# Kernel optimization log

Hardware: AMD Instinct MI355X
Metric: run time of the kernel (lower is better)

## Reference

```python
import jax, jax.numpy as jnp
import numpy as np
from jax import lax

NLAT_IN, NLON_IN = 480, 960
NLAT_OUT, NLON_OUT = 721, 1440
KSIZE = 9      # morlet basis: prod(kernel_shape) = 3*3
NNZ = 20       # sparse quadrature entries per output latitude row
C_IN, C_OUT = 32, 32
BATCH = 1


def setup_inputs() -> dict:
    key = jax.random.key(0)
    k1, k2, k3, k4, k5 = jax.random.split(key, 5)
    x = jax.random.normal(k1, (BATCH, C_IN, NLAT_IN, NLON_IN), dtype=jnp.float32)
    weight = jax.random.normal(k2, (C_OUT, C_IN, KSIZE), dtype=jnp.float32) * 0.05
    # sparse DISCO quadrature values (quadrature weights folded in)
    psi_vals = jax.random.uniform(k3, (KSIZE, NLAT_OUT, NNZ), dtype=jnp.float32) / NNZ
    # geodesic neighborhood: latitude rows within +-2 of output row, small lon offsets
    ho = jnp.arange(NLAT_OUT, dtype=jnp.int32)[:, None]
    psi_hi = jnp.clip(ho + jax.random.randint(k4, (NLAT_OUT, NNZ), -2, 3, dtype=jnp.int32), 0, NLAT_OUT - 1)
    psi_dw = jax.random.randint(k5, (NLAT_OUT, NNZ), -10, 11, dtype=jnp.int32) % NLON_OUT
    return {"x": x, "weight": weight, "psi_vals": psi_vals, "psi_hi": psi_hi, "psi_dw": psi_dw}


def _resample_s2(x, h_out, w_out):
    """Bilinear lat interpolation + periodic linear lon interpolation (ResampleS2)."""
    b, c, h, w = x.shape
    # latitude: both grids are linspace(0, pi, nlat) equiangular
    pos_h = jnp.linspace(0.0, float(h - 1), h_out)
    h0 = jnp.clip(jnp.floor(pos_h).astype(jnp.int32), 0, h - 2)
    fh = (pos_h - h0.astype(jnp.float32)).astype(x.dtype)
    x = x[:, :, h0, :] * (1.0 - fh)[None, None, :, None] + x[:, :, h0 + 1, :] * fh[None, None, :, None]
    # longitude: periodic, lon_j = 2*pi*j/nlon
    pos_w = jnp.arange(w_out, dtype=jnp.float32) * (w / w_out)
    w0 = jnp.floor(pos_w).astype(jnp.int32)
    fw = (pos_w - w0.astype(jnp.float32)).astype(x.dtype)
    w0 = w0 % w
    w1 = (w0 + 1) % w
    return x[..., w0] * (1.0 - fw) + x[..., w1] * fw


def _disco_conv(x, weight, psi_vals, psi_hi, psi_dw):
    """Sparse discrete-continuous spherical conv (gather -> basis weight -> channel mix).
    psi is stored for longitude 0 and applied with a periodic longitude shift."""
    b, c, h, w = x.shape  # [B, Cin, 721, 1440]
    o = weight.shape[0]
    wo = jnp.arange(w, dtype=jnp.int32)

    def body(acc, inp):
        v, hi, dw = inp  # v: [K, Hout], hi/dw: [Hout]
        cols = (dw[:, None] + wo[None, :]) % w          # [Hout, W]
        g = x[:, :, hi[:, None], cols]                  # gather -> [B, Cin, Hout, W]
        weff = jnp.einsum("ock,kh->och", weight, v)     # fold basis into channel mix
        return acc + jnp.einsum("och,bchw->bohw", weff, g), None

    acc0 = jnp.zeros((b, o, h, w), dtype=x.dtype)
    scan_in = (jnp.moveaxis(psi_vals, 2, 0), psi_hi.T, psi_dw.T)  # leading axis NNZ
    acc, _ = lax.scan(body, acc0, scan_in)
    return acc


def reference(x, weight, psi_vals, psi_hi, psi_dw):
    x = _resample_s2(x, NLAT_OUT, NLON_OUT)
    return _disco_conv(x, weight, psi_vals, psi_hi, psi_dw)
```

## Files before the change

### kernel.cpp

```cpp
#include <hip/hip_runtime.h>
#include <hip/hip_bf16.h>

#define NLAT_IN  480
#define NLON_IN  960
#define NLAT_OUT 721
#define NLON_OUT 1440
#define KSIZE    9
#define NNZ      20
#define CH       32

typedef __bf16 bf16x8 __attribute__((ext_vector_type(8)));
typedef float  f32x4  __attribute__((ext_vector_type(4)));

__device__ __forceinline__ unsigned short f2bf(float f) {
    unsigned u = __float_as_uint(f);
    u += 0x7fffu + ((u >> 16) & 1u);
    return (unsigned short)(u >> 16);
}

#define W_TILE   180
#define IN_LD4   31
#define LDS_PITCH 129

__global__ __launch_bounds__(256) void resample_kernel(
        const float* __restrict__ x,
        unsigned short* __restrict__ xr) {
    __shared__ float ld[2 * CH * LDS_PITCH];

    int h  = blockIdx.y;
    int bx = blockIdx.x;
    int wb = bx * W_TILE;
    int base_in = bx * (W_TILE * 2 / 3);

    float pos_h = (float)h * (479.0f / 720.0f);
    int h0 = (int)floorf(pos_h);
    if (h0 < 0) h0 = 0;
    if (h0 > NLAT_IN - 2) h0 = NLAT_IN - 2;
    float fh = pos_h - (float)h0;

    const int t = threadIdx.x;
    for (int i = 0; i < 8; ++i) {
        int lin = i * 256 + t;
        if (lin < 2 * CH * IN_LD4) {
            int r   = lin / (CH * IN_LD4);
            int rem = lin - r * (CH * IN_LD4);
            int c   = rem / IN_LD4;
            int j   = rem - c * IN_LD4;
            int src = base_in + 4 * j;
            if (src >= NLON_IN) src -= NLON_IN;
            f32x4 v = *(const f32x4*)(x + ((size_t)c * NLAT_IN + h0 + r) * NLON_IN + src);
            float* dst = ld + (r * CH + c) * LDS_PITCH + 4 * j;
            dst[0] = v.x; dst[1] = v.y; dst[2] = v.z; dst[3] = v.w;
        }
    }
    __syncthreads();

    float ifh = 1.0f - fh;
    for (int i = 0; i < 12; ++i) {
        int d = i * 256 + t;
        if (d >= W_TILE * (CH / 2)) break;
        int w_l   = d >> 4;
        int cpair = d & 15;
        int c = cpair * 2;
        int w = wb + w_l;
        float pos_w = (float)w * ((float)NLON_IN / (float)NLON_OUT);
        int w0 = (int)floorf(pos_w);
        float fw = pos_w - (float)w0;
        int wl0 = w0 - base_in;
        float ifw = 1.0f - fw;

        const float* r0 = ld + c * LDS_PITCH + wl0;
        const float* r1 = r0 + CH * LDS_PITCH;
        float v0 = ifh * (ifw * r0[0] + fw * r0[1]) + fh * (ifw * r1[0] + fw * r1[1]);
        const float* q0 = r0 + LDS_PITCH;
        const float* q1 = r1 + LDS_PITCH;
        float v1 = ifh * (ifw * q0[0] + fw * q0[1]) + fh * (ifw * q1[0] + fw * q1[1]);

        ((unsigned*)xr)[((size_t)h * NLON_OUT + w) * (CH / 2) + cpair] =
            (unsigned)f2bf(v0) | ((unsigned)f2bf(v1) << 16);
    }
}

__global__ __launch_bounds__(256) void weff_kernel(
        const float* __restrict__ weight,
        const float* __restrict__ psi_vals,
        unsigned short* __restrict__ weff) {
    __shared__ float wl[KSIZE * CH * CH];

    const int t = threadIdx.x;
    for (int i = 0; i < 9; ++i) {
        int lin = i * 256 + t;
        if (lin < KSIZE * CH * CH / 4) {
            f32x4 v = *(const f32x4*)(weight + lin * 4);
            float vv[4] = {v.x, v.y, v.z, v.w};
#pragma unroll
            for (int q = 0; q < 4; ++q) {
                int l4 = lin * 4 + q;
                int k  = l4 % KSIZE;
                int occ = l4 / KSIZE;
                wl[k * (CH * CH) + occ] = vv[q];
            }
        }
    }
    __syncthreads();

    int hnz = blockIdx.x * 16 + (t >> 4);
    int cp  = t & 15;
    if (hnz >= NLAT_OUT * NNZ) return;

    float p[KSIZE];
#pragma unroll
    for (int k = 0; k < KSIZE; ++k)
        p[k] = psi_vals[(size_t)k * (NLAT_OUT * NNZ) + hnz];

    unsigned* outp = (unsigned*)weff + (size_t)hnz * (CH * CH / 2) + cp;
#pragma unroll 4
    for (int oc = 0; oc < CH; ++oc) {
        float a0 = 0.f, a1 = 0.f;
        const float* wb = wl + oc * CH + cp * 2;
#pragma unroll
        for (int k = 0; k < KSIZE; ++k) {
            a0 += wb[k * (CH * CH)]     * p[k];
            a1 += wb[k * (CH * CH) + 1] * p[k];
        }
        outp[oc * 16] = (unsigned)f2bf(a0) | ((unsigned)f2bf(a1) << 16);
    }
}

#define ST_ROWS 6
#define ST_COLS 128
#define HBLK2   361
#define NPAIR   (HBLK2 * 15)
#define PER_XCD ((NPAIR + 7) / 8)

__global__ __launch_bounds__(256, 3) void disco_kernel(
        const unsigned short* __restrict__ xr,
        const unsigned short* __restrict__ weff,
        const int* __restrict__ psi_hi,
        const int* __restrict__ psi_dw,
        float* __restrict__ out) {
    __shared__ unsigned short st[ST_ROWS * ST_COLS * CH];

    int bid = blockIdx.x;
    int xcd = bid & 7;
    int p   = xcd * PER_XCD + (bid >> 3);
    if (p >= NPAIR) return;
    int hblk = p / 15;
    int wblk = p - hblk * 15;
    int h0        = hblk * 2;
    int wbase_blk = wblk * 96;

    int wave = threadIdx.x >> 6;
    int lane = threadIdx.x & 63;
    int l15  = lane & 15;
    int quad = lane >> 4;
    int c0   = quad * 8;
    int jh   = wave >> 1;
    int wq   = wave & 1;

    int cstart = wbase_blk - 16;
    if (cstart < 0) cstart += NLON_OUT;
    for (int i = wave; i < ST_ROWS * (ST_COLS / 16); i += 4) {
        int r  = i >> 3;
        int ck = i & 7;
        int gh = h0 - 2 + r;
        gh = gh < 0 ? 0 : (gh > NLAT_OUT - 1 ? NLAT_OUT - 1 : gh);
        int gc = cstart + ck * 16;
        if (gc >= NLON_OUT) gc -= NLON_OUT;
        const unsigned short* gp = xr + ((size_t)gh * NLON_OUT + gc) * CH + lane * 8;
        unsigned short* lp = st + (r * ST_COLS + ck * 16) * CH;
        __builtin_amdgcn_global_load_lds(
            (const __attribute__((address_space(1))) void*)gp,
            (__attribute__((address_space(3))) void*)lp, 16, 0, 0);
    }
    __syncthreads();

    int h = h0 + jh;
    if (h < NLAT_OUT) {
        f32x4 acc[2][3] = {};
        const unsigned short* weff_h = weff + (size_t)h * (NNZ * CH * CH);
        const int* hip_ = psi_hi + h * NNZ;
        const int* dwp  = psi_dw + h * NNZ;
        int wcol0 = 16 + wq * 48 + l15;

#pragma unroll 2
        for (int nz = 0; nz < NNZ; ++nz) {
            int hi = hip_[nz];
            int dw = dwp[nz];
            int shift = dw > 720 ? dw - NLON_OUT : dw;
            int rloc  = hi - h0 + 2;
            const unsigned short* wf = weff_h + nz * (CH * CH);
            bf16x8 a0 = *(const bf16x8*)(wf + l15 * CH + c0);
            bf16x8 a1 = *(const bf16x8*)(wf + (16 + l15) * CH + c0);
            const unsigned short* srow = st + (size_t)rloc * (ST_COLS * CH);
            int cbase = wcol0 + shift;
#pragma unroll
            for (int s = 0; s < 3; ++s) {
                bf16x8 b = *(const bf16x8*)(srow + (cbase + s * 16) * CH + c0);
                acc[0][s] = __builtin_amdgcn_mfma_f32_16x16x32_bf16(a0, b, acc[0][s], 0, 0, 0);
                acc[1][s] = __builtin_amdgcn_mfma_f32_16x16x32_bf16(a1, b, acc[1][s], 0, 0, 0);
            }
        }

#pragma unroll
        for (int hh = 0; hh < 2; ++hh)
#pragma unroll
            for (int s = 0; s < 3; ++s)
#pragma unroll
                for (int r = 0; r < 4; ++r) {
                    int oc = hh * 16 + quad * 4 + r;
                    int w  = wbase_blk + wq * 48 + s * 16 + l15;
                    out[((size_t)oc * NLAT_OUT + h) * NLON_OUT + w] = acc[hh][s][r];
                }
    }
}

extern "C" void kernel_launch(void* const* d_in, const int* in_sizes, int n_in,
                              void* d_out, int out_size, void* d_ws, size_t ws_size,
                              hipStream_t stream) {
    const float* x        = (const float*)d_in[0];
    const float* weight   = (const float*)d_in[1];
    const float* psi_vals = (const float*)d_in[2];
    const int*   psi_hi   = (const int*)d_in[3];
    const int*   psi_dw   = (const int*)d_in[4];
    float* out = (float*)d_out;

    unsigned short* xr = (unsigned short*)d_ws;
    unsigned short* wf = (unsigned short*)((char*)d_ws + (size_t)NLAT_OUT * NLON_OUT * CH * 2);

    {
        dim3 grid(NLON_OUT / W_TILE, NLAT_OUT);
        resample_kernel<<<grid, 256, 0, stream>>>(x, xr);
    }
    {
        int nblk = (NLAT_OUT * NNZ + 15) / 16;
        weff_kernel<<<nblk, 256, 0, stream>>>(weight, psi_vals, wf);
    }
    {
        disco_kernel<<<8 * PER_XCD, 256, 0, stream>>>(xr, wf, psi_hi, psi_dw, out);
    }
}
```

Measured before the change: 316.5 us.

## Widen disco tiles to four rows, swizzle LDS, prefetch weff, vectorize resample stores

The disco kernel now processes four output latitude rows per block using 512 threads. Its staged halo grows from 6 to 8 rows, so each staged input row is reused by more output rows. LDS staging uses an XOR swizzle on column-group offsets to cut bank conflicts on the B-operand reads. Weff fragments and psi indices are software-prefetched two iterations ahead with the nz loop fully unrolled. The resample kernel writes 16-byte vectors of eight channels per thread instead of 4-byte pairs. The trade-off is more registers and LDS per block, which may lower occupancy.

```diff
diff --git a/kernel.cpp b/kernel.cpp
--- a/kernel.cpp
+++ b/kernel.cpp
@@ -11,6 +11,7 @@
 
 typedef __bf16 bf16x8 __attribute__((ext_vector_type(8)));
 typedef float  f32x4  __attribute__((ext_vector_type(4)));
+typedef unsigned u32x4 __attribute__((ext_vector_type(4)));
 
 __device__ __forceinline__ unsigned short f2bf(float f) {
     unsigned u = __float_as_uint(f);
@@ -56,12 +57,11 @@
     __syncthreads();
 
     float ifh = 1.0f - fh;
-    for (int i = 0; i < 12; ++i) {
+    for (int i = 0; i < 3; ++i) {
         int d = i * 256 + t;
-        if (d >= W_TILE * (CH / 2)) break;
-        int w_l   = d >> 4;
-        int cpair = d & 15;
-        int c = cpair * 2;
+        if (d >= W_TILE * (CH / 8)) break;
+        int w_l = d >> 2;
+        int cg  = d & 3;
         int w = wb + w_l;
         float pos_w = (float)w * ((float)NLON_IN / (float)NLON_OUT);
         int w0 = (int)floorf(pos_w);
@@ -69,15 +69,20 @@
         int wl0 = w0 - base_in;
         float ifw = 1.0f - fw;
 
-        const float* r0 = ld + c * LDS_PITCH + wl0;
-        const float* r1 = r0 + CH * LDS_PITCH;
-        float v0 = ifh * (ifw * r0[0] + fw * r0[1]) + fh * (ifw * r1[0] + fw * r1[1]);
-        const float* q0 = r0 + LDS_PITCH;
-        const float* q1 = r1 + LDS_PITCH;
-        float v1 = ifh * (ifw * q0[0] + fw * q0[1]) + fh * (ifw * q1[0] + fw * q1[1]);
-
-        ((unsigned*)xr)[((size_t)h * NLON_OUT + w) * (CH / 2) + cpair] =
-            (unsigned)f2bf(v0) | ((unsigned)f2bf(v1) << 16);
+        unsigned rr[4];
+#pragma unroll
+        for (int j = 0; j < 4; ++j) {
+            int c = cg * 8 + j * 2;
+            const float* r0 = ld + c * LDS_PITCH + wl0;
+            const float* r1 = r0 + CH * LDS_PITCH;
+            float v0 = ifh * (ifw * r0[0] + fw * r0[1]) + fh * (ifw * r1[0] + fw * r1[1]);
+            const float* q0 = r0 + LDS_PITCH;
+            const float* q1 = r1 + LDS_PITCH;
+            float v1 = ifh * (ifw * q0[0] + fw * q0[1]) + fh * (ifw * q1[0] + fw * q1[1]);
+            rr[j] = (unsigned)f2bf(v0) | ((unsigned)f2bf(v1) << 16);
+        }
+        u32x4 uv; uv[0] = rr[0]; uv[1] = rr[1]; uv[2] = rr[2]; uv[3] = rr[3];
+        *(u32x4*)((unsigned*)xr + ((size_t)h * NLON_OUT + w) * (CH / 2) + cg * 4) = uv;
     }
 }
 
@@ -127,13 +132,13 @@
     }
 }
 
-#define ST_ROWS 6
+#define ST_ROWS 8
 #define ST_COLS 128
-#define HBLK2   361
-#define NPAIR   (HBLK2 * 15)
-#define PER_XCD ((NPAIR + 7) / 8)
-
-__global__ __launch_bounds__(256, 3) void disco_kernel(
+#define HBLK4   181
+#define NPAIRD  (HBLK4 * 15)
+#define PER_XCD ((NPAIRD + 7) / 8)
+
+__global__ __launch_bounds__(512, 4) void disco_kernel(
         const unsigned short* __restrict__ xr,
         const unsigned short* __restrict__ weff,
         const int* __restrict__ psi_hi,
@@ -144,10 +149,10 @@
     int bid = blockIdx.x;
     int xcd = bid & 7;
     int p   = xcd * PER_XCD + (bid >> 3);
-    if (p >= NPAIR) return;
+    if (p >= NPAIRD) return;
     int hblk = p / 15;
     int wblk = p - hblk * 15;
-    int h0        = hblk * 2;
+    int h0        = hblk * 4;
     int wbase_blk = wblk * 96;
 
     int wave = threadIdx.x >> 6;
@@ -158,16 +163,38 @@
     int jh   = wave >> 1;
     int wq   = wave & 1;
 
+    int  h  = h0 + jh;
+    bool hv = (h < NLAT_OUT);
+
+    int swz = ((lane >> 2) << 5) + (((lane & 3) ^ ((lane >> 3) & 3)) << 3);
+
+    const unsigned short* weff_h = weff + (size_t)h * (NNZ * CH * CH);
+    const int* hip_ = psi_hi + h * NNZ;
+    const int* dwp  = psi_dw + h * NNZ;
+
+    bf16x8 pa0[2], pa1[2];
+    int phi[2], pdw[2];
+    if (hv) {
+#pragma unroll
+        for (int q = 0; q < 2; ++q) {
+            const unsigned short* wp = weff_h + q * (CH * CH);
+            pa0[q] = *(const bf16x8*)(wp + l15 * CH + c0);
+            pa1[q] = *(const bf16x8*)(wp + (16 + l15) * CH + c0);
+            phi[q] = hip_[q];
+            pdw[q] = dwp[q];
+        }
+    }
+
     int cstart = wbase_blk - 16;
     if (cstart < 0) cstart += NLON_OUT;
-    for (int i = wave; i < ST_ROWS * (ST_COLS / 16); i += 4) {
+    for (int i = wave; i < ST_ROWS * (ST_COLS / 16); i += 8) {
         int r  = i >> 3;
         int ck = i & 7;
         int gh = h0 - 2 + r;
         gh = gh < 0 ? 0 : (gh > NLAT_OUT - 1 ? NLAT_OUT - 1 : gh);
         int gc = cstart + ck * 16;
         if (gc >= NLON_OUT) gc -= NLON_OUT;
-        const unsigned short* gp = xr + ((size_t)gh * NLON_OUT + gc) * CH + lane * 8;
+        const unsigned short* gp = xr + ((size_t)gh * NLON_OUT + gc) * CH + swz;
         unsigned short* lp = st + (r * ST_COLS + ck * 16) * CH;
         __builtin_amdgcn_global_load_lds(
             (const __attribute__((address_space(1))) void*)gp,
@@ -175,28 +202,33 @@
     }
     __syncthreads();
 
-    int h = h0 + jh;
-    if (h < NLAT_OUT) {
+    if (hv) {
         f32x4 acc[2][3] = {};
-        const unsigned short* weff_h = weff + (size_t)h * (NNZ * CH * CH);
-        const int* hip_ = psi_hi + h * NNZ;
-        const int* dwp  = psi_dw + h * NNZ;
         int wcol0 = 16 + wq * 48 + l15;
 
-#pragma unroll 2
+#pragma unroll
         for (int nz = 0; nz < NNZ; ++nz) {
-            int hi = hip_[nz];
-            int dw = dwp[nz];
+            const int sl = nz & 1;
+            bf16x8 a0 = pa0[sl];
+            bf16x8 a1 = pa1[sl];
+            int hi = phi[sl];
+            int dw = pdw[sl];
+            if (nz + 2 < NNZ) {
+                const unsigned short* wp = weff_h + (nz + 2) * (CH * CH);
+                pa0[sl] = *(const bf16x8*)(wp + l15 * CH + c0);
+                pa1[sl] = *(const bf16x8*)(wp + (16 + l15) * CH + c0);
+                phi[sl] = hip_[nz + 2];
+                pdw[sl] = dwp[nz + 2];
+            }
             int shift = dw > 720 ? dw - NLON_OUT : dw;
             int rloc  = hi - h0 + 2;
-            const unsigned short* wf = weff_h + nz * (CH * CH);
-            bf16x8 a0 = *(const bf16x8*)(wf + l15 * CH + c0);
-            bf16x8 a1 = *(const bf16x8*)(wf + (16 + l15) * CH + c0);
-            const unsigned short* srow = st + (size_t)rloc * (ST_COLS * CH);
             int cbase = wcol0 + shift;
+            int sel   = ((((cbase >> 1) & 3) ^ quad) << 3);
+            const unsigned short* bp =
+                st + (size_t)rloc * (ST_COLS * CH) + cbase * CH + sel;
 #pragma unroll
             for (int s = 0; s < 3; ++s) {
-                bf16x8 b = *(const bf16x8*)(srow + (cbase + s * 16) * CH + c0);
+                bf16x8 b = *(const bf16x8*)(bp + s * 16 * CH);
                 acc[0][s] = __builtin_amdgcn_mfma_f32_16x16x32_bf16(a0, b, acc[0][s], 0, 0, 0);
                 acc[1][s] = __builtin_amdgcn_mfma_f32_16x16x32_bf16(a1, b, acc[1][s], 0, 0, 0);
             }
@@ -237,6 +269,6 @@
         weff_kernel<<<nblk, 256, 0, stream>>>(weight, psi_vals, wf);
     }
     {
-        disco_kernel<<<8 * PER_XCD, 256, 0, stream>>>(xr, wf, psi_hi, psi_dw, out);
-    }
-}
+        disco_kernel<<<8 * PER_XCD, 512, 0, stream>>>(xr, wf, psi_hi, psi_dw, out);
+    }
+}
```

New measurement: 305.6 us. 1.04x faster.
